# Optimization experiments

Hardware: AMD Instinct MI355X
Metric: run time of the kernel (lower is better)

## Reference

```python
import jax, jax.numpy as jnp
import numpy as np

WIDTH = 768
HEAD = 64

def setup_inputs() -> dict:
    key = jax.random.key(0)
    ks = jax.random.split(key, 8)
    x = jax.random.normal(ks[0], (8, 2048, WIDTH), dtype=jnp.float32)
    mask = jax.random.randint(ks[1], (2048, 2048), 0, 2, dtype=jnp.int32)
    s = 1.0 / np.sqrt(WIDTH)
    Wq = jax.random.normal(ks[2], (WIDTH, HEAD), dtype=jnp.float32) * s
    Wk = jax.random.normal(ks[3], (WIDTH, HEAD), dtype=jnp.float32) * s
    Wv = jax.random.normal(ks[4], (WIDTH, HEAD), dtype=jnp.float32) * s
    bq = jax.random.normal(ks[5], (HEAD,), dtype=jnp.float32) * 0.01
    bk = jax.random.normal(ks[6], (HEAD,), dtype=jnp.float32) * 0.01
    bv = jax.random.normal(ks[7], (HEAD,), dtype=jnp.float32) * 0.01
    return {"x": x, "Wq": Wq, "bq": bq, "Wk": Wk, "bk": bk, "Wv": Wv, "bv": bv, "mask": mask}

def reference(x, Wq, bq, Wk, bk, Wv, bv, mask) -> jnp.ndarray:
    # x: [B, N, width]; projections -> [B, N, head]
    Q = jnp.einsum('bnw,wh->bnh', x, Wq) + bq
    K = jnp.einsum('bnw,wh->bnh', x, Wk) + bk
    V = jnp.einsum('bnw,wh->bnh', x, Wv) + bv
    scale = 1.0 / jnp.sqrt(jnp.asarray(Q.shape[-1], dtype=Q.dtype))
    scores = jnp.einsum('bqh,bkh->bqk', Q, K) * scale  # [B, N, N]
    scores = jnp.where(mask == 0, -jnp.inf, scores)
    attn = jax.nn.softmax(scores, axis=-1)
    return jnp.einsum('bqk,bkh->bqh', attn, V)
```

## Files before the change

### kernel.cpp

```cpp
#include <hip/hip_runtime.h>

typedef short  s8v   __attribute__((ext_vector_type(8)));
typedef float  f32x4 __attribute__((ext_vector_type(4)));

#define SEQ 2048
#define WID 768

__device__ __forceinline__ unsigned fbits(float f) {
    union { float f; unsigned u; } v; v.f = f; return v.u;
}
__device__ __forceinline__ float bitsf(unsigned u) {
    union { unsigned u; float f; } v; v.u = u; return v.f;
}
__device__ __forceinline__ unsigned short f2b(float f) {
    unsigned u = fbits(f);
    return (unsigned short)((u + 0x7FFFu + ((u >> 16) & 1u)) >> 16);
}
__device__ __forceinline__ unsigned packRNE(float a, float b) {
    unsigned ta = fbits(a) + 0x7FFFu + ((fbits(a) >> 16) & 1u);
    unsigned tb = fbits(b) + 0x7FFFu + ((fbits(b) >> 16) & 1u);
    return __builtin_amdgcn_perm(tb, ta, 0x07060302u);
}
__device__ __forceinline__ unsigned packTRUNC(float a, float b) {
    return __builtin_amdgcn_perm(fbits(b), fbits(a), 0x07060302u);
}
__device__ __forceinline__ f32x4 zero4() { f32x4 z = {0.f, 0.f, 0.f, 0.f}; return z; }

__device__ __forceinline__ void async16(const unsigned short* g, unsigned short* l) {
    __builtin_amdgcn_global_load_lds(
        (const __attribute__((address_space(1))) unsigned int*)g,
        (__attribute__((address_space(3))) unsigned int*)l, 16, 0, 0);
}

__global__ __launch_bounds__(256) void convert_kernel(
    const int* __restrict__ mask,
    const float* __restrict__ Wq, const float* __restrict__ Wk, const float* __restrict__ Wv,
    unsigned short* __restrict__ WF, unsigned* __restrict__ PM)
{
    const int tid = threadIdx.x;
    const int blk = blockIdx.x;
    if (blk < 512) {
        const int gid  = blk * 4 + (tid >> 6);
        const int lane = tid & 63, quad = lane >> 4, c = lane & 15;
        const int qb = gid >> 5, kb = gid & 31;
        unsigned w = 0;
        #pragma unroll
        for (int mt = 0; mt < 2; ++mt) {
            const int q = qb * 32 + mt * 16 + c;
            #pragma unroll
            for (int i = 0; i < 4; ++i) {
                const int4 mm = *(const int4*)&mask[(size_t)q * SEQ + kb * 64 + quad * 16 + 4 * i];
                if (mm.x) w |= 1u << (mt * 16 + i * 4 + 0);
                if (mm.y) w |= 1u << (mt * 16 + i * 4 + 1);
                if (mm.z) w |= 1u << (mt * 16 + i * 4 + 2);
                if (mm.w) w |= 1u << (mt * 16 + i * 4 + 3);
            }
        }
        PM[(size_t)gid * 64 + lane] = w;
    } else {
        const int s2 = (blk - 512) * 256 + tid;
        const int chunk = s2 >> 6, l = s2 & 63;
        const int ntg = chunk / 24, r = chunk - ntg * 24;
        const int kc = r >> 1, h = r & 1;
        const int mat = ntg >> 2;
        const int col = (ntg & 3) * 16 + (l & 15);
        const int k0 = kc * 64 + h * 32 + (l >> 4) * 8;
        const float* Wm = (mat == 0) ? Wq : (mat == 1) ? Wk : Wv;
        float p[8];
        #pragma unroll
        for (int j = 0; j < 8; ++j) p[j] = Wm[(size_t)(k0 + j) * 64 + col];
        uint4 w;
        w.x = packRNE(p[0], p[1]); w.y = packRNE(p[2], p[3]);
        w.z = packRNE(p[4], p[5]); w.w = packRNE(p[6], p[7]);
        *(uint4*)&WF[(size_t)s2 * 8] = w;
    }
}

__global__ __launch_bounds__(1024, 2) void fused_pa(
    const float* __restrict__ x, const unsigned short* __restrict__ WF,
    const float* __restrict__ bq, const float* __restrict__ bk, const float* __restrict__ bv,
    const unsigned* __restrict__ PM,
    unsigned short* __restrict__ QF, unsigned short* __restrict__ KF,
    unsigned short* __restrict__ VF, float* __restrict__ out,
    unsigned* __restrict__ bar)
{
    __shared__ __align__(16) unsigned char SMEM[65536];

    const int tid = threadIdx.x;
    const int wv = tid >> 6, lane = tid & 63, quad = lane >> 4, c = lane & 15;
    const int blk = blockIdx.x;

    {
        unsigned short (*AB)[16384] = (unsigned short(*)[16384])SMEM;
        unsigned short (*St)[200]   = (unsigned short(*)[200])SMEM;
        const int g0 = blk * 4;
        const int rg = wv >> 2, cg = wv & 3;

        float bias[3];
        #pragma unroll
        for (int nt = 0; nt < 3; ++nt) {
            int col = cg * 48 + nt * 16 + c;
            const float* B = (col < 64) ? bq : (col < 128) ? bk : bv;
            bias[nt] = B[col & 63];
        }

        const int ach = tid >> 7;
        const int agl = ach >> 1, ah = ach & 1;
        const int al  = (tid >> 1) & 63;
        const int aj0 = (tid & 1) * 4;
        const float* xptr = x + (size_t)((g0 + agl) * 16 + (al & 15)) * WID
                              + ah * 32 + (al >> 4) * 8 + aj0;

        auto issueB = [&](int kc, int b) {
            if (wv < 12) {
                #pragma unroll
                for (int r = 0; r < 2; ++r) {
                    const int e = wv * 2 + r;
                    const int ntg = e >> 1, h = e & 1;
                    async16(WF + (((size_t)ntg * 12 + kc) * 2 + h) * 512 + lane * 8,
                            &AB[b][4096 + (ntg * 2 + h) * 512]);
                }
            }
        };
        auto stageA = [&](int b, float4 f) {
            uint2 w2;
            w2.x = packRNE(f.x, f.y);
            w2.y = packRNE(f.z, f.w);
            *(uint2*)&AB[b][(size_t)tid * 4] = w2;
        };

        f32x4 acc[3];
        #pragma unroll
        for (int nt = 0; nt < 3; ++nt) acc[nt] = zero4();

        {
            float4 f = *(const float4*)&xptr[0];
            stageA(0, f);
            issueB(0, 0);
        }

        for (int kc = 0; kc < 12; ++kc) {
            const int b = kc & 1;
            __syncthreads();
            float4 f;
            if (kc < 11) {
                f = *(const float4*)&xptr[(kc + 1) * 64];
                issueB(kc + 1, b ^ 1);
            }

            s8v afr[2], bfr[3][2];
            #pragma unroll
            for (int h = 0; h < 2; ++h)
                afr[h] = *(const s8v*)&AB[b][(rg * 2 + h) * 512 + lane * 8];
            #pragma unroll
            for (int nt = 0; nt < 3; ++nt)
                #pragma unroll
                for (int h = 0; h < 2; ++h)
                    bfr[nt][h] = *(const s8v*)&AB[b][4096 + ((cg * 3 + nt) * 2 + h) * 512 + lane * 8];
            #pragma unroll
            for (int h = 0; h < 2; ++h)
                #pragma unroll
                for (int nt = 0; nt < 3; ++nt)
                    acc[nt] = __builtin_amdgcn_mfma_f32_16x16x32_bf16(
                        afr[h], bfr[nt][h], acc[nt], 0, 0, 0);

            if (kc < 11) stageA(b ^ 1, f);
        }

        #pragma unroll
        for (int nt = 0; nt < 3; ++nt)
            #pragma unroll
            for (int i = 0; i < 4; ++i)
                St[rg * 16 + quad * 4 + i][cg * 48 + nt * 16 + c]
                    = f2b(acc[nt][i] + bias[nt]);
        __syncthreads();

        if (tid < 512) {
            const int g = tid >> 7, ks = (tid >> 6) & 1, l = tid & 63;
            uint4 v = *(uint4*)&St[g * 16 + (l & 15)][ks * 32 + (l >> 4) * 8];
            *(uint4*)&QF[(((size_t)(g0 + g)) * 2 + ks) * 512 + (size_t)l * 8] = v;
        } else {
            const int t2 = tid - 512;
            const int ksnt = t2 >> 6, l = t2 & 63;
            const int ks = ksnt >> 2, nt = ksnt & 3;
            uint4 v = *(uint4*)&St[4 * (l & 15) + nt][64 + ks * 32 + (l >> 4) * 8];
            *(uint4*)&KF[(((size_t)blk * 8 + ksnt) * 64 + l) * 8] = v;
        }
        if (tid < 512) {
            const int ksnt = tid >> 6, l = tid & 63;
            const int ks = ksnt >> 2, nt = ksnt & 3;
            const int d = 128 + nt * 16 + (l & 15);
            const int r0 = (l >> 4) * 16 + ks * 8;
            unsigned short p[8];
            #pragma unroll
            for (int s = 0; s < 8; ++s) p[s] = St[r0 + s][d];
            uint4 w;
            w.x = (unsigned)p[0] | ((unsigned)p[1] << 16);
            w.y = (unsigned)p[2] | ((unsigned)p[3] << 16);
            w.z = (unsigned)p[4] | ((unsigned)p[5] << 16);
            w.w = (unsigned)p[6] | ((unsigned)p[7] << 16);
            *(uint4*)&VF[(((size_t)blk * 8 + ksnt) * 64 + l) * 8] = w;
        }
    }

    __syncthreads();
    if (tid == 0) {
        __threadfence();
        atomicAdd(&bar[blk >> 5], 1u);
        while (atomicAdd(&bar[blk & 7], 0u) < 32u)
            __builtin_amdgcn_s_sleep(2);
    }
    __syncthreads();

    {
        float (*Obuf)[68] = (float(*)[68])SMEM;
        float* Lbuf       = (float*)(SMEM + 17408);

        const int sl = wv & 3, qg = wv >> 2, mt = qg & 1;
        const int bb = blk & 7, qt = blk >> 3;
        const size_t qrow0 = (size_t)bb * SEQ + qt * 64;

        if (tid < 64) Lbuf[tid] = 0.f;

        union Q8 { s8v v; unsigned w[4]; } qf[2];
        {
            const size_t qgrp = (size_t)bb * 128 + qt * 4 + qg;
            #pragma unroll
            for (int ks = 0; ks < 2; ++ks)
                qf[ks].v = *(const s8v*)&QF[(qgrp * 2 + ks) * 512 + (size_t)lane * 8];
        }

        f32x4 O[4];
        float lro0 = 0.f, lro1 = 0.f;
        #pragma unroll
        for (int nt = 0; nt < 4; ++nt) O[nt] = zero4();

        const unsigned* pmrow = PM + (size_t)((qt * 2 + (qg >> 1)) * 32 + sl * 8) * 64 + lane;

        #pragma unroll 1
        for (int kt = 0; kt < 8; ++kt) {
            const size_t kbg = (size_t)bb * 32 + sl * 8 + kt;
            const unsigned short* kb_ = KF + kbg * 4096 + (size_t)lane * 8;
            const unsigned short* vb_ = VF + kbg * 4096 + (size_t)lane * 8;

            const unsigned pmw = pmrow[(size_t)kt * 64];

            s8v vfr[8];
            #pragma unroll
            for (int d = 0; d < 8; ++d) vfr[d] = *(const s8v*)&vb_[(size_t)d * 512];
            s8v kfr[8];
            #pragma unroll
            for (int d = 0; d < 8; ++d) kfr[d] = *(const s8v*)&kb_[(size_t)d * 512];

            f32x4 S[4];
            #pragma unroll
            for (int nt = 0; nt < 4; ++nt) S[nt] = zero4();
            #pragma unroll
            for (int ks = 0; ks < 2; ++ks)
                #pragma unroll
                for (int nt = 0; nt < 4; ++nt)
                    S[nt] = __builtin_amdgcn_mfma_f32_16x16x32_bf16(kfr[ks * 4 + nt], qf[ks].v, S[nt], 0, 0, 0);

            const unsigned pmh = pmw >> (mt * 16);
            float p[4][4];
            #pragma unroll
            for (int i = 0; i < 4; ++i)
                #pragma unroll
                for (int nt = 0; nt < 4; ++nt) {
                    float e = exp2f(fmaf(S[nt][i], 0.18033688011112042f, -21.640425613334451f));
                    p[nt][i] = ((pmh >> (i * 4 + nt)) & 1u) ? e : 0.f;
                }
            union { unsigned w[8]; s8v v[2]; } P;
            #pragma unroll
            for (int j = 0; j < 8; ++j) {
                unsigned uu = packTRUNC(p[2 * (j & 1)][j >> 1], p[2 * (j & 1) + 1][j >> 1]);
                P.w[j] = uu;
                if (j & 1) lro1 += bitsf(uu << 16) + bitsf(uu & 0xFFFF0000u);
                else       lro0 += bitsf(uu << 16) + bitsf(uu & 0xFFFF0000u);
            }

            #pragma unroll
            for (int ks = 0; ks < 2; ++ks)
                #pragma unroll
                for (int nt = 0; nt < 4; ++nt)
                    O[nt] = __builtin_amdgcn_mfma_f32_16x16x32_bf16(P.v[ks], vfr[ks * 4 + nt], O[nt], 0, 0, 0);
        }

        #pragma unroll
        for (int j = 0; j < 5; ++j) {
            int idx = tid + 1024 * j;
            if (idx < 64 * 68) ((float*)Obuf)[idx] = 0.f;
        }
        __syncthreads();

        {
            float l = lro0 + lro1;
            l += __shfl_xor(l, 16);
            l += __shfl_xor(l, 32);
            if (quad == 0) atomicAdd(&Lbuf[qg * 16 + c], l);
        }
        #pragma unroll
        for (int i = 0; i < 4; ++i)
            #pragma unroll
            for (int nt = 0; nt < 4; ++nt)
                atomicAdd(&Obuf[qg * 16 + quad * 4 + i][nt * 16 + c], O[nt][i]);
        __syncthreads();
        {
            const int r = tid >> 4, d4 = (tid & 15) * 4;
            const float invL = 1.0f / Lbuf[r];
            float4 v = *(float4*)&Obuf[r][d4];
            float4 o = make_float4(v.x * invL, v.y * invL, v.z * invL, v.w * invL);
            *(float4*)&out[(qrow0 + r) * 64 + d4] = o;
        }
    }
}

extern "C" void kernel_launch(void* const* d_in, const int* in_sizes, int n_in,
                              void* d_out, int out_size, void* d_ws, size_t ws_size,
                              hipStream_t stream)
{
    const float* x    = (const float*)d_in[0];
    const float* Wq   = (const float*)d_in[1];
    const float* bq   = (const float*)d_in[2];
    const float* Wk   = (const float*)d_in[3];
    const float* bk   = (const float*)d_in[4];
    const float* Wv   = (const float*)d_in[5];
    const float* bv   = (const float*)d_in[6];
    const int*   mask = (const int*)d_in[7];
    float* out = (float*)d_out;

    unsigned short* QF = (unsigned short*)d_ws;
    unsigned short* KF = QF + (size_t)16384 * 64;
    unsigned short* VF = KF + (size_t)16384 * 64;
    unsigned short* WF = VF + (size_t)16384 * 64;
    unsigned*       PM = (unsigned*)(WF + (size_t)192 * WID);
    unsigned*       bar = PM + (size_t)2048 * 64;

    hipMemsetAsync(bar, 0, 32, stream);
    convert_kernel<<<584, 256, 0, stream>>>(mask, Wq, Wk, Wv, WF, PM);
    fused_pa<<<256, 1024, 0, stream>>>(x, WF, bq, bk, bv, PM, QF, KF, VF, out, bar);
}
```

Measured before the change: 172.1 us.

## Split fused persistent kernel into separate projection and attention kernels

Replaces the single fused kernel, which used a global atomic spin barrier between the QKV projection and the attention phases, with two kernel launches. The projection kernel now loads x and the weight fragments straight from global memory into registers instead of double-buffering them in LDS with async loads. The attention kernel uses 512 blocks of 32 query rows each, which halves per-block work and LDS so more blocks can be resident. This removes the spin barrier and the memset, at the cost of an extra launch and the loss of LDS-staged reuse in the projection.

```diff
diff --git a/kernel.cpp b/kernel.cpp
--- a/kernel.cpp
+++ b/kernel.cpp
@@ -25,12 +25,6 @@
     return __builtin_amdgcn_perm(fbits(b), fbits(a), 0x07060302u);
 }
 __device__ __forceinline__ f32x4 zero4() { f32x4 z = {0.f, 0.f, 0.f, 0.f}; return z; }
-
-__device__ __forceinline__ void async16(const unsigned short* g, unsigned short* l) {
-    __builtin_amdgcn_global_load_lds(
-        (const __attribute__((address_space(1))) unsigned int*)g,
-        (__attribute__((address_space(3))) unsigned int*)l, 16, 0, 0);
-}
 
 __global__ __launch_bounds__(256) void convert_kernel(
     const int* __restrict__ mask,
@@ -76,242 +70,204 @@
     }
 }
 
-__global__ __launch_bounds__(1024, 2) void fused_pa(
+__global__ __launch_bounds__(1024, 4) void qkv_proj_kernel(
     const float* __restrict__ x, const unsigned short* __restrict__ WF,
     const float* __restrict__ bq, const float* __restrict__ bk, const float* __restrict__ bv,
-    const unsigned* __restrict__ PM,
     unsigned short* __restrict__ QF, unsigned short* __restrict__ KF,
-    unsigned short* __restrict__ VF, float* __restrict__ out,
-    unsigned* __restrict__ bar)
-{
-    __shared__ __align__(16) unsigned char SMEM[65536];
+    unsigned short* __restrict__ VF)
+{
+    __shared__ unsigned short St[64][200];
 
     const int tid = threadIdx.x;
     const int wv = tid >> 6, lane = tid & 63, quad = lane >> 4, c = lane & 15;
+    const int rg = wv >> 2, cg = wv & 3;
     const int blk = blockIdx.x;
-
+    const int g0 = blk * 4;
+
+    float bias[3];
+    #pragma unroll
+    for (int nt = 0; nt < 3; ++nt) {
+        int col = cg * 48 + nt * 16 + c;
+        const float* B = (col < 64) ? bq : (col < 128) ? bk : bv;
+        bias[nt] = B[col & 63];
+    }
+
+    const float* xA = x + (size_t)((g0 + rg) * 16 + c) * WID + quad * 8;
+
+    f32x4 acc[3];
+    #pragma unroll
+    for (int nt = 0; nt < 3; ++nt) acc[nt] = zero4();
+
+    #pragma unroll 1
+    for (int kc = 0; kc < 12; ++kc) {
+        s8v bfr[3][2];
+        #pragma unroll
+        for (int nt = 0; nt < 3; ++nt)
+            #pragma unroll
+            for (int h = 0; h < 2; ++h)
+                bfr[nt][h] = *(const s8v*)&WF[(((size_t)(cg * 3 + nt) * 12 + kc) * 2 + h) * 512 + lane * 8];
+
+        s8v afr[2];
+        #pragma unroll
+        for (int h = 0; h < 2; ++h) {
+            float4 f0 = *(const float4*)&xA[kc * 64 + h * 32];
+            float4 f1 = *(const float4*)&xA[kc * 64 + h * 32 + 4];
+            union { uint4 u; s8v v; } w;
+            w.u.x = packRNE(f0.x, f0.y); w.u.y = packRNE(f0.z, f0.w);
+            w.u.z = packRNE(f1.x, f1.y); w.u.w = packRNE(f1.z, f1.w);
+            afr[h] = w.v;
+        }
+
+        #pragma unroll
+        for (int h = 0; h < 2; ++h)
+            #pragma unroll
+            for (int nt = 0; nt < 3; ++nt)
+                acc[nt] = __builtin_amdgcn_mfma_f32_16x16x32_bf16(
+                    afr[h], bfr[nt][h], acc[nt], 0, 0, 0);
+    }
+
+    #pragma unroll
+    for (int nt = 0; nt < 3; ++nt)
+        #pragma unroll
+        for (int i = 0; i < 4; ++i)
+            St[rg * 16 + quad * 4 + i][cg * 48 + nt * 16 + c]
+                = f2b(acc[nt][i] + bias[nt]);
+    __syncthreads();
+
+    if (tid < 512) {
+        const int g = tid >> 7, ks = (tid >> 6) & 1, l = tid & 63;
+        uint4 v = *(uint4*)&St[g * 16 + (l & 15)][ks * 32 + (l >> 4) * 8];
+        *(uint4*)&QF[(((size_t)(g0 + g)) * 2 + ks) * 512 + (size_t)l * 8] = v;
+    } else {
+        const int t2 = tid - 512;
+        const int ksnt = t2 >> 6, l = t2 & 63;
+        const int ks = ksnt >> 2, nt = ksnt & 3;
+        uint4 v = *(uint4*)&St[4 * (l & 15) + nt][64 + ks * 32 + (l >> 4) * 8];
+        *(uint4*)&KF[(((size_t)blk * 8 + ksnt) * 64 + l) * 8] = v;
+    }
+    if (tid < 512) {
+        const int ksnt = tid >> 6, l = tid & 63;
+        const int ks = ksnt >> 2, nt = ksnt & 3;
+        const int d = 128 + nt * 16 + (l & 15);
+        const int r0 = (l >> 4) * 16 + ks * 8;
+        unsigned short p[8];
+        #pragma unroll
+        for (int s = 0; s < 8; ++s) p[s] = St[r0 + s][d];
+        uint4 w;
+        w.x = (unsigned)p[0] | ((unsigned)p[1] << 16);
+        w.y = (unsigned)p[2] | ((unsigned)p[3] << 16);
+        w.z = (unsigned)p[4] | ((unsigned)p[5] << 16);
+        w.w = (unsigned)p[6] | ((unsigned)p[7] << 16);
+        *(uint4*)&VF[(((size_t)blk * 8 + ksnt) * 64 + l) * 8] = w;
+    }
+}
+
+__global__ __launch_bounds__(1024, 8) void attn_kernel(
+    const unsigned short* __restrict__ QF, const unsigned short* __restrict__ KF,
+    const unsigned short* __restrict__ VF, const unsigned* __restrict__ PM,
+    float* __restrict__ out)
+{
+    __shared__ float Obuf[32][68];
+    __shared__ float Lbuf[32];
+
+    const int tid = threadIdx.x;
+    const int wv = tid >> 6, lane = tid & 63, quad = lane >> 4, c = lane & 15;
+    const int sl = wv & 7, qg = wv >> 3;
+    const int blk = blockIdx.x;
+    const int bb = blk & 7, qt = blk >> 3;
+    const size_t qrow0 = (size_t)bb * SEQ + qt * 32;
+
+    if (tid < 32) Lbuf[tid] = 0.f;
+
+    union Q8 { s8v v; unsigned w[4]; } qf[2];
     {
-        unsigned short (*AB)[16384] = (unsigned short(*)[16384])SMEM;
-        unsigned short (*St)[200]   = (unsigned short(*)[200])SMEM;
-        const int g0 = blk * 4;
-        const int rg = wv >> 2, cg = wv & 3;
-
-        float bias[3];
-        #pragma unroll
-        for (int nt = 0; nt < 3; ++nt) {
-            int col = cg * 48 + nt * 16 + c;
-            const float* B = (col < 64) ? bq : (col < 128) ? bk : bv;
-            bias[nt] = B[col & 63];
+        const size_t qgrp = (size_t)bb * 128 + qt * 2 + qg;
+        #pragma unroll
+        for (int ks = 0; ks < 2; ++ks)
+            qf[ks].v = *(const s8v*)&QF[(qgrp * 2 + ks) * 512 + (size_t)lane * 8];
+    }
+
+    f32x4 O[4];
+    float lro0 = 0.f, lro1 = 0.f;
+    #pragma unroll
+    for (int nt = 0; nt < 4; ++nt) O[nt] = zero4();
+
+    const unsigned* pmrow = PM + (size_t)(qt * 32 + sl * 4) * 64 + lane;
+
+    #pragma unroll 1
+    for (int kt = 0; kt < 4; ++kt) {
+        const size_t kbg = (size_t)bb * 32 + sl * 4 + kt;
+        const unsigned short* kb_ = KF + kbg * 4096 + (size_t)lane * 8;
+        const unsigned short* vb_ = VF + kbg * 4096 + (size_t)lane * 8;
+
+        const unsigned pmw = pmrow[(size_t)kt * 64];
+
+        s8v vfr[8];
+        #pragma unroll
+        for (int d = 0; d < 8; ++d) vfr[d] = *(const s8v*)&vb_[(size_t)d * 512];
+        s8v kfr[8];
+        #pragma unroll
+        for (int d = 0; d < 8; ++d) kfr[d] = *(const s8v*)&kb_[(size_t)d * 512];
+
+        f32x4 S[4];
+        #pragma unroll
+        for (int nt = 0; nt < 4; ++nt) S[nt] = zero4();
+        #pragma unroll
+        for (int ks = 0; ks < 2; ++ks)
+            #pragma unroll
+            for (int nt = 0; nt < 4; ++nt)
+                S[nt] = __builtin_amdgcn_mfma_f32_16x16x32_bf16(kfr[ks * 4 + nt], qf[ks].v, S[nt], 0, 0, 0);
+
+        const unsigned pmh = pmw >> (qg * 16);
+        float p[4][4];
+        #pragma unroll
+        for (int i = 0; i < 4; ++i)
+            #pragma unroll
+            for (int nt = 0; nt < 4; ++nt) {
+                float e = exp2f(fmaf(S[nt][i], 0.18033688011112042f, -21.640425613334451f));
+                p[nt][i] = ((pmh >> (i * 4 + nt)) & 1u) ? e : 0.f;
+            }
+        union { unsigned w[8]; s8v v[2]; } P;
+        #pragma unroll
+        for (int j = 0; j < 8; ++j) {
+            unsigned uu = packTRUNC(p[2 * (j & 1)][j >> 1], p[2 * (j & 1) + 1][j >> 1]);
+            P.w[j] = uu;
+            if (j & 1) lro1 += bitsf(uu << 16) + bitsf(uu & 0xFFFF0000u);
+            else       lro0 += bitsf(uu << 16) + bitsf(uu & 0xFFFF0000u);
         }
 
-        const int ach = tid >> 7;
-        const int agl = ach >> 1, ah = ach & 1;
-        const int al  = (tid >> 1) & 63;
-        const int aj0 = (tid & 1) * 4;
-        const float* xptr = x + (size_t)((g0 + agl) * 16 + (al & 15)) * WID
-                              + ah * 32 + (al >> 4) * 8 + aj0;
-
-        auto issueB = [&](int kc, int b) {
-            if (wv < 12) {
-                #pragma unroll
-                for (int r = 0; r < 2; ++r) {
-                    const int e = wv * 2 + r;
-                    const int ntg = e >> 1, h = e & 1;
-                    async16(WF + (((size_t)ntg * 12 + kc) * 2 + h) * 512 + lane * 8,
-                            &AB[b][4096 + (ntg * 2 + h) * 512]);
-                }
-            }
-        };
-        auto stageA = [&](int b, float4 f) {
-            uint2 w2;
-            w2.x = packRNE(f.x, f.y);
-            w2.y = packRNE(f.z, f.w);
-            *(uint2*)&AB[b][(size_t)tid * 4] = w2;
-        };
-
-        f32x4 acc[3];
-        #pragma unroll
-        for (int nt = 0; nt < 3; ++nt) acc[nt] = zero4();
-
-        {
-            float4 f = *(const float4*)&xptr[0];
-            stageA(0, f);
-            issueB(0, 0);
-        }
-
-        for (int kc = 0; kc < 12; ++kc) {
-            const int b = kc & 1;
-            __syncthreads();
-            float4 f;
-            if (kc < 11) {
-                f = *(const float4*)&xptr[(kc + 1) * 64];
-                issueB(kc + 1, b ^ 1);
-            }
-
-            s8v afr[2], bfr[3][2];
-            #pragma unroll
-            for (int h = 0; h < 2; ++h)
-                afr[h] = *(const s8v*)&AB[b][(rg * 2 + h) * 512 + lane * 8];
-            #pragma unroll
-            for (int nt = 0; nt < 3; ++nt)
-                #pragma unroll
-                for (int h = 0; h < 2; ++h)
-                    bfr[nt][h] = *(const s8v*)&AB[b][4096 + ((cg * 3 + nt) * 2 + h) * 512 + lane * 8];
-            #pragma unroll
-            for (int h = 0; h < 2; ++h)
-                #pragma unroll
-                for (int nt = 0; nt < 3; ++nt)
-                    acc[nt] = __builtin_amdgcn_mfma_f32_16x16x32_bf16(
-                        afr[h], bfr[nt][h], acc[nt], 0, 0, 0);
-
-            if (kc < 11) stageA(b ^ 1, f);
-        }
-
-        #pragma unroll
-        for (int nt = 0; nt < 3; ++nt)
-            #pragma unroll
-            for (int i = 0; i < 4; ++i)
-                St[rg * 16 + quad * 4 + i][cg * 48 + nt * 16 + c]
-                    = f2b(acc[nt][i] + bias[nt]);
-        __syncthreads();
-
-        if (tid < 512) {
-            const int g = tid >> 7, ks = (tid >> 6) & 1, l = tid & 63;
-            uint4 v = *(uint4*)&St[g * 16 + (l & 15)][ks * 32 + (l >> 4) * 8];
-            *(uint4*)&QF[(((size_t)(g0 + g)) * 2 + ks) * 512 + (size_t)l * 8] = v;
-        } else {
-            const int t2 = tid - 512;
-            const int ksnt = t2 >> 6, l = t2 & 63;
-            const int ks = ksnt >> 2, nt = ksnt & 3;
-            uint4 v = *(uint4*)&St[4 * (l & 15) + nt][64 + ks * 32 + (l >> 4) * 8];
-            *(uint4*)&KF[(((size_t)blk * 8 + ksnt) * 64 + l) * 8] = v;
-        }
-        if (tid < 512) {
-            const int ksnt = tid >> 6, l = tid & 63;
-            const int ks = ksnt >> 2, nt = ksnt & 3;
-            const int d = 128 + nt * 16 + (l & 15);
-            const int r0 = (l >> 4) * 16 + ks * 8;
-            unsigned short p[8];
-            #pragma unroll
-            for (int s = 0; s < 8; ++s) p[s] = St[r0 + s][d];
-            uint4 w;
-            w.x = (unsigned)p[0] | ((unsigned)p[1] << 16);
-            w.y = (unsigned)p[2] | ((unsigned)p[3] << 16);
-            w.z = (unsigned)p[4] | ((unsigned)p[5] << 16);
-            w.w = (unsigned)p[6] | ((unsigned)p[7] << 16);
-            *(uint4*)&VF[(((size_t)blk * 8 + ksnt) * 64 + l) * 8] = w;
-        }
-    }
-
+        #pragma unroll
+        for (int ks = 0; ks < 2; ++ks)
+            #pragma unroll
+            for (int nt = 0; nt < 4; ++nt)
+                O[nt] = __builtin_amdgcn_mfma_f32_16x16x32_bf16(P.v[ks], vfr[ks * 4 + nt], O[nt], 0, 0, 0);
+    }
+
+    #pragma unroll
+    for (int j = 0; j < 3; ++j) {
+        int idx = tid + 1024 * j;
+        if (idx < 32 * 68) ((float*)Obuf)[idx] = 0.f;
+    }
     __syncthreads();
-    if (tid == 0) {
-        __threadfence();
-        atomicAdd(&bar[blk >> 5], 1u);
-        while (atomicAdd(&bar[blk & 7], 0u) < 32u)
-            __builtin_amdgcn_s_sleep(2);
-    }
+
+    {
+        float l = lro0 + lro1;
+        l += __shfl_xor(l, 16);
+        l += __shfl_xor(l, 32);
+        if (quad == 0) atomicAdd(&Lbuf[qg * 16 + c], l);
+    }
+    #pragma unroll
+    for (int i = 0; i < 4; ++i)
+        #pragma unroll
+        for (int nt = 0; nt < 4; ++nt)
+            atomicAdd(&Obuf[qg * 16 + quad * 4 + i][nt * 16 + c], O[nt][i]);
     __syncthreads();
-
-    {
-        float (*Obuf)[68] = (float(*)[68])SMEM;
-        float* Lbuf       = (float*)(SMEM + 17408);
-
-        const int sl = wv & 3, qg = wv >> 2, mt = qg & 1;
-        const int bb = blk & 7, qt = blk >> 3;
-        const size_t qrow0 = (size_t)bb * SEQ + qt * 64;
-
-        if (tid < 64) Lbuf[tid] = 0.f;
-
-        union Q8 { s8v v; unsigned w[4]; } qf[2];
-        {
-            const size_t qgrp = (size_t)bb * 128 + qt * 4 + qg;
-            #pragma unroll
-            for (int ks = 0; ks < 2; ++ks)
-                qf[ks].v = *(const s8v*)&QF[(qgrp * 2 + ks) * 512 + (size_t)lane * 8];
-        }
-
-        f32x4 O[4];
-        float lro0 = 0.f, lro1 = 0.f;
-        #pragma unroll
-        for (int nt = 0; nt < 4; ++nt) O[nt] = zero4();
-
-        const unsigned* pmrow = PM + (size_t)((qt * 2 + (qg >> 1)) * 32 + sl * 8) * 64 + lane;
-
-        #pragma unroll 1
-        for (int kt = 0; kt < 8; ++kt) {
-            const size_t kbg = (size_t)bb * 32 + sl * 8 + kt;
-            const unsigned short* kb_ = KF + kbg * 4096 + (size_t)lane * 8;
-            const unsigned short* vb_ = VF + kbg * 4096 + (size_t)lane * 8;
-
-            const unsigned pmw = pmrow[(size_t)kt * 64];
-
-            s8v vfr[8];
-            #pragma unroll
-            for (int d = 0; d < 8; ++d) vfr[d] = *(const s8v*)&vb_[(size_t)d * 512];
-            s8v kfr[8];
-            #pragma unroll
-            for (int d = 0; d < 8; ++d) kfr[d] = *(const s8v*)&kb_[(size_t)d * 512];
-
-            f32x4 S[4];
-            #pragma unroll
-            for (int nt = 0; nt < 4; ++nt) S[nt] = zero4();
-            #pragma unroll
-            for (int ks = 0; ks < 2; ++ks)
-                #pragma unroll
-                for (int nt = 0; nt < 4; ++nt)
-                    S[nt] = __builtin_amdgcn_mfma_f32_16x16x32_bf16(kfr[ks * 4 + nt], qf[ks].v, S[nt], 0, 0, 0);
-
-            const unsigned pmh = pmw >> (mt * 16);
-            float p[4][4];
-            #pragma unroll
-            for (int i = 0; i < 4; ++i)
-                #pragma unroll
-                for (int nt = 0; nt < 4; ++nt) {
-                    float e = exp2f(fmaf(S[nt][i], 0.18033688011112042f, -21.640425613334451f));
-                    p[nt][i] = ((pmh >> (i * 4 + nt)) & 1u) ? e : 0.f;
-                }
-            union { unsigned w[8]; s8v v[2]; } P;
-            #pragma unroll
-            for (int j = 0; j < 8; ++j) {
-                unsigned uu = packTRUNC(p[2 * (j & 1)][j >> 1], p[2 * (j & 1) + 1][j >> 1]);
-                P.w[j] = uu;
-                if (j & 1) lro1 += bitsf(uu << 16) + bitsf(uu & 0xFFFF0000u);
-                else       lro0 += bitsf(uu << 16) + bitsf(uu & 0xFFFF0000u);
-            }
-
-            #pragma unroll
-            for (int ks = 0; ks < 2; ++ks)
-                #pragma unroll
-                for (int nt = 0; nt < 4; ++nt)
-                    O[nt] = __builtin_amdgcn_mfma_f32_16x16x32_bf16(P.v[ks], vfr[ks * 4 + nt], O[nt], 0, 0, 0);
-        }
-
-        #pragma unroll
-        for (int j = 0; j < 5; ++j) {
-            int idx = tid + 1024 * j;
-            if (idx < 64 * 68) ((float*)Obuf)[idx] = 0.f;
-        }
-        __syncthreads();
-
-        {
-            float l = lro0 + lro1;
-            l += __shfl_xor(l, 16);
-            l += __shfl_xor(l, 32);
-            if (quad == 0) atomicAdd(&Lbuf[qg * 16 + c], l);
-        }
-        #pragma unroll
-        for (int i = 0; i < 4; ++i)
-            #pragma unroll
-            for (int nt = 0; nt < 4; ++nt)
-                atomicAdd(&Obuf[qg * 16 + quad * 4 + i][nt * 16 + c], O[nt][i]);
-        __syncthreads();
-        {
-            const int r = tid >> 4, d4 = (tid & 15) * 4;
-            const float invL = 1.0f / Lbuf[r];
-            float4 v = *(float4*)&Obuf[r][d4];
-            float4 o = make_float4(v.x * invL, v.y * invL, v.z * invL, v.w * invL);
-            *(float4*)&out[(qrow0 + r) * 64 + d4] = o;
-        }
+    if (tid < 512) {
+        const int r = tid >> 4, d4 = (tid & 15) * 4;
+        const float invL = 1.0f / Lbuf[r];
+        float4 v = *(float4*)&Obuf[r][d4];
+        float4 o = make_float4(v.x * invL, v.y * invL, v.z * invL, v.w * invL);
+        *(float4*)&out[(qrow0 + r) * 64 + d4] = o;
     }
 }
 
@@ -334,9 +290,8 @@
     unsigned short* VF = KF + (size_t)16384 * 64;
     unsigned short* WF = VF + (size_t)16384 * 64;
     unsigned*       PM = (unsigned*)(WF + (size_t)192 * WID);
-    unsigned*       bar = PM + (size_t)2048 * 64;
-
-    hipMemsetAsync(bar, 0, 32, stream);
+
     convert_kernel<<<584, 256, 0, stream>>>(mask, Wq, Wk, Wv, WF, PM);
-    fused_pa<<<256, 1024, 0, stream>>>(x, WF, bq, bk, bv, PM, QF, KF, VF, out, bar);
-}
+    qkv_proj_kernel<<<256, 1024, 0, stream>>>(x, WF, bq, bk, bv, QF, KF, VF);
+    attn_kernel<<<512, 1024, 0, stream>>>(QF, KF, VF, PM, out);
+}
```

After: 208.4 us. +21.1%, slower.
